# Kernel optimization log

Hardware: AMD Instinct MI355X
Metric: run time of the kernel (lower is better)

The kernel has to match this reference:

```python
import jax, jax.numpy as jnp
import numpy as np

B, S, D = 2, 2048, 1024
H, DK = 16, 64            # num_heads, d_kv; inner_dim = H*DK = 1024
NUM_BUCKETS = 32
MAX_DISTANCE = 128


def _relative_position_bucket(relative_position, bidirectional=True,
                              num_buckets=NUM_BUCKETS, max_distance=MAX_DISTANCE):
    # Faithful port of Mesh-TF / HF T5 bucketing (int32 in, int32 buckets out).
    relative_buckets = jnp.zeros_like(relative_position)
    if bidirectional:
        num_buckets = num_buckets // 2
        relative_buckets = relative_buckets + (relative_position > 0).astype(jnp.int32) * num_buckets
        relative_position = jnp.abs(relative_position)
    else:
        relative_position = -jnp.minimum(relative_position, 0)
    max_exact = num_buckets // 2
    is_small = relative_position < max_exact
    # log-spaced buckets for large distances; guard log(0) (masked by is_small anyway)
    rel_f = jnp.maximum(relative_position, 1).astype(jnp.float32)
    val_if_large = max_exact + (
        jnp.log(rel_f / max_exact) / np.log(max_distance / max_exact) * (num_buckets - max_exact)
    ).astype(jnp.int32)
    val_if_large = jnp.minimum(val_if_large, num_buckets - 1)
    return relative_buckets + jnp.where(is_small, relative_position, val_if_large)


def compute_bias(rel_emb, query_length, key_length):
    ctx = jnp.arange(query_length, dtype=jnp.int32)[:, None]
    mem = jnp.arange(key_length, dtype=jnp.int32)[None, :]
    buckets = _relative_position_bucket(mem - ctx, bidirectional=True)  # [q, k]
    values = rel_emb[buckets]                       # [q, k, H]
    return jnp.transpose(values, (2, 0, 1))[None]   # [1, H, q, k]


def setup_inputs() -> dict:
    key = jax.random.key(0)
    ks = jax.random.split(key, 6)
    scale = 1.0 / np.sqrt(D)
    return {
        "hidden_states": jax.random.normal(ks[0], (B, S, D), jnp.float32),
        "wq": jax.random.normal(ks[1], (D, H * DK), jnp.float32) * scale,
        "wk": jax.random.normal(ks[2], (D, H * DK), jnp.float32) * scale,
        "wv": jax.random.normal(ks[3], (D, H * DK), jnp.float32) * scale,
        "wo": jax.random.normal(ks[4], (H * DK, D), jnp.float32) * scale,
        "rel_emb": jax.random.normal(ks[5], (NUM_BUCKETS, H), jnp.float32),
    }


def reference(hidden_states, wq, wk, wv, wo, rel_emb):
    b, s, _ = hidden_states.shape

    def shape(x):  # [B,S,H*DK] -> [B,H,S,DK]
        return x.reshape(b, s, H, DK).transpose(0, 2, 1, 3)

    q = shape(hidden_states @ wq)   # NOTE: T5 does not scale q by 1/sqrt(d_kv)
    k = shape(hidden_states @ wk)
    v = shape(hidden_states @ wv)

    scores = jnp.einsum("bhqd,bhkd->bhqk", q, k)
    position_bias = compute_bias(rel_emb, s, s)     # [1,H,S,S]
    scores = scores + position_bias
    attn = jax.nn.softmax(scores, axis=-1)
    ctx = jnp.einsum("bhqk,bhkd->bhqd", attn, v)    # [B,H,S,DK]
    ctx = ctx.transpose(0, 2, 1, 3).reshape(b, s, H * DK)
    return ctx @ wo
```

## Files before the change

kernel.cpp:

```cpp
#include <hip/hip_runtime.h>


typedef __attribute__((ext_vector_type(8)))  unsigned short u16x8;
typedef __attribute__((ext_vector_type(4)))  unsigned short u16x4;
typedef __attribute__((ext_vector_type(8)))  __bf16         bf16x8;
typedef __attribute__((ext_vector_type(4)))  float          f32x4;
typedef __attribute__((ext_vector_type(4)))  unsigned int   u32x4;

#define GLOBAL_AS __attribute__((address_space(1)))
#define LDS_AS    __attribute__((address_space(3)))

static __device__ inline f32x4 MFMA(u16x8 a, u16x8 b, f32x4 c) {
  return __builtin_amdgcn_mfma_f32_16x16x32_bf16(
      __builtin_bit_cast(bf16x8, a), __builtin_bit_cast(bf16x8, b), c, 0, 0, 0);
}

static __device__ inline void gload16(const void* g, void* l) {
  __builtin_amdgcn_global_load_lds((const GLOBAL_AS unsigned int*)g,
                                   (LDS_AS unsigned int*)l, 16, 0, 0);
}

static __device__ inline unsigned short f2bf(float x) {
  unsigned int u = __builtin_bit_cast(unsigned int, x);
  u = (u + 0x7FFFu + ((u >> 16) & 1u)) >> 16;
  return (unsigned short)u;
}

static __device__ inline unsigned int cvtpk(float lo, float hi) {
  unsigned int r;
  asm volatile("v_cvt_pk_bf16_f32 %0, %1, %2" : "=v"(r) : "v"(lo), "v"(hi));
  return r;
}

static __device__ inline float max3f(float a, float b, float c) {
  float r;
  asm volatile("v_max3_f32 %0, %1, %2, %3" : "=v"(r) : "v"(a), "v"(b), "v"(c));
  return r;
}

#define L2E 1.4426950408889634f

__global__ __launch_bounds__(256) void k_prep(const float* __restrict__ hs,
                                              const float* __restrict__ wq,
                                              const float* __restrict__ wk,
                                              const float* __restrict__ wv,
                                              const float* __restrict__ wo,
                                              const float* __restrict__ re,
                                              unsigned short* __restrict__ hsb,
                                              unsigned short* __restrict__ wt,
                                              unsigned short* __restrict__ wot,
                                              float* __restrict__ btab) {
  __shared__ float tile[64][65];
  const int bid = blockIdx.x;
  const int t = threadIdx.x;

  if (bid < 4096) {
    int i = bid * 256 + t;
    float4 v = *(const float4*)(hs + (size_t)i * 4);
    u16x4 o;
    o[0] = f2bf(v.x); o[1] = f2bf(v.y); o[2] = f2bf(v.z); o[3] = f2bf(v.w);
    *(u16x4*)(hsb + (size_t)i * 4) = o;
  } else if (bid < 5120) {
    int sub = bid - 4096;
    int which = sub >> 8;
    int sb = sub & 255;
    int n0 = (sb & 15) << 6, k0 = (sb >> 4) << 6;
    const float* src = which == 0 ? wq : which == 1 ? wk : which == 2 ? wv : wo;
    unsigned short* dst = which == 0 ? wt
                        : which == 1 ? wt + 1048576
                        : which == 2 ? wt + 2097152 : wot;
    const int K = 1024, N = 1024;
    int rr = t >> 4, cc = (t & 15) << 2;
#pragma unroll
    for (int j = 0; j < 4; j++) {
      float4 v = *(const float4*)(src + (size_t)(k0 + rr + j * 16) * N + n0 + cc);
      tile[rr + j * 16][cc + 0] = v.x;
      tile[rr + j * 16][cc + 1] = v.y;
      tile[rr + j * 16][cc + 2] = v.z;
      tile[rr + j * 16][cc + 3] = v.w;
    }
    __syncthreads();
#pragma unroll
    for (int j = 0; j < 4; j++) {
      int n = rr + j * 16;
      u16x4 o;
      o[0] = f2bf(tile[cc + 0][n]);
      o[1] = f2bf(tile[cc + 1][n]);
      o[2] = f2bf(tile[cc + 2][n]);
      o[3] = f2bf(tile[cc + 3][n]);
      *(u16x4*)(dst + (size_t)(n0 + n) * K + k0 + cc) = o;
    }
  } else {
    int i = (bid - 5120) * 256 + t;
    if (i < 16 * 4095) {
      int h = i / 4095;
      int rp = i % 4095 - 2047;
      int rb = rp > 0 ? 16 : 0;
      int arp = rp < 0 ? -rp : rp;
      int v;
      if (arp < 8) {
        v = arp;
      } else {
        float tt = logf((float)arp * 0.125f);
        tt = tt / 2.772588722239781f;
        tt = tt * 8.0f;
        v = 8 + (int)tt;
        if (v > 15) v = 15;
      }
      btab[i] = re[(rb + v) * 16 + h] * L2E;
    }
  }
}

template <int EPI>
__global__ __launch_bounds__(256) void k_gemm(const unsigned short* __restrict__ A,
                                              const unsigned short* __restrict__ Bt,
                                              void* __restrict__ outp,
                                              int M, int N, int K) {
  __shared__ __attribute__((aligned(16))) char smem[32768];
  const int tid = threadIdx.x;
  const int lane = tid & 63, w = tid >> 6;
  const int l15 = lane & 15, g = lane >> 4;
  const int wr = w >> 1, wc = w & 1;
  const int bm0 = blockIdx.y << 7, bn0 = blockIdx.x << 7;

  const char* Ag = (const char*)A + (size_t)bm0 * K * 2;
  const char* Bg = (const char*)Bt + (size_t)bn0 * K * 2;

  f32x4 acc[4][4];
#pragma unroll
  for (int i = 0; i < 4; i++)
#pragma unroll
    for (int j = 0; j < 4; j++) acc[i][j] = (f32x4)0.0f;

  const int rowA = wr * 64 + l15;
  const int rowB = wc * 64 + l15;
  const int swz = (l15 & 7) << 4;

  for (int kt = 0; kt < K; kt += 64) {
#pragma unroll
    for (int j = 0; j < 4; j++) {
      int idx = ((j * 4 + w) << 10) + (lane << 4);
      int row = idx >> 7;
      int gs = (idx >> 4) & 7;
      size_t co = (size_t)row * (K * 2) + kt * 2 + ((gs ^ (row & 7)) << 4);
      gload16(Ag + co, smem + ((j * 4 + w) << 10));
      gload16(Bg + co, smem + 16384 + ((j * 4 + w) << 10));
    }
    __syncthreads();
#pragma unroll
    for (int kk = 0; kk < 2; kk++) {
      const int cp = ((kk << 6) + (g << 4)) ^ swz;
      u16x8 af[4], bfv[4];
#pragma unroll
      for (int mt = 0; mt < 4; mt++)
        af[mt] = *(const u16x8*)(smem + ((rowA + mt * 16) << 7) + cp);
#pragma unroll
      for (int nt = 0; nt < 4; nt++)
        bfv[nt] = *(const u16x8*)(smem + 16384 + ((rowB + nt * 16) << 7) + cp);
#pragma unroll
      for (int mt = 0; mt < 4; mt++)
#pragma unroll
        for (int nt = 0; nt < 4; nt++)
          acc[mt][nt] = MFMA(af[mt], bfv[nt], acc[mt][nt]);
    }
    __syncthreads();
  }

#pragma unroll
  for (int mt = 0; mt < 4; mt++) {
#pragma unroll
    for (int nt = 0; nt < 4; nt++) {
#pragma unroll
      for (int r = 0; r < 4; r++) {
        int m = bm0 + wr * 64 + mt * 16 + g * 4 + r;
        int n = bn0 + wc * 64 + nt * 16 + l15;
        float val = acc[mt][nt][r];
        if (EPI == 0) {
          int which = n >> 10;
          int hh = (n >> 6) & 15;
          int d = n & 63;
          int bb = m >> 11, s = m & 2047;
          int plane = bb * 16 + hh;
          unsigned short* o = (unsigned short*)outp;
          if (which == 0) {
            o[(size_t)plane * 131072 + (size_t)s * 64 + d] = f2bf(val * L2E);
          } else if (which == 1) {
            o[4194304 + (size_t)plane * 131072 + (size_t)s * 64 + d] = f2bf(val);
          } else {
            o[8388608 + (size_t)plane * 131072 + (size_t)d * 2048 + s] = f2bf(val);
          }
        } else {
          ((float*)outp)[(size_t)m * N + n] = val;
        }
      }
    }
  }
}

__global__ __launch_bounds__(256, 2) void k_attn(const unsigned short* __restrict__ qkv,
                                                 const float* __restrict__ btab,
                                                 unsigned short* __restrict__ ctx) {
  __shared__ __attribute__((aligned(16))) char smem[65536];
  const int tid = threadIdx.x;
  const int lane = tid & 63, w = tid >> 6;
  const int l15 = lane & 15, g = lane >> 4;

  const int wg = ((blockIdx.x & 7) << 6) + (blockIdx.x >> 3);
  const int plane = wg >> 4, qb = wg & 15;
  const int h = plane & 15, b = plane >> 4;
  const int q0w = (qb << 7) + (w << 5);

  const unsigned short* Qp = qkv + (size_t)plane * 131072;
  const unsigned short* Kp = qkv + 4194304 + (size_t)plane * 131072;
  const unsigned short* Vt = qkv + 8388608 + (size_t)plane * 131072;

  u16x8 qaA[2], qaB[2];
#pragma unroll
  for (int kk = 0; kk < 2; kk++) {
    qaA[kk] = *(const u16x8*)(Qp + (size_t)(q0w + l15) * 64 + kk * 32 + g * 8);
    qaB[kk] = *(const u16x8*)(Qp + (size_t)(q0w + 16 + l15) * 64 + kk * 32 + g * 8);
  }

  float m_rA = 0.0f, m_rB = 0.0f;
  f32x4 oaccA[4], oaccB[4], laccA, laccB;
#pragma unroll
  for (int t = 0; t < 4; t++) { oaccA[t] = (f32x4)0.0f; oaccB[t] = (f32x4)0.0f; }
  laccA = (f32x4)0.0f; laccB = (f32x4)0.0f;

  const float* browA = btab + h * 4095 + 2047 - q0w;
  const float* browB = browA - 16;
  const float cpos = btab[h * 4095 + 2047 + 1024];
  const float cneg = btab[h * 4095 + 2047 - 1024];

  u16x8 ones;
  {
    u32x4 ov = {0x3F803F80u, 0x3F803F80u, 0x3F803F80u, 0x3F803F80u};
    ones = __builtin_bit_cast(u16x8, ov);
  }

  const int srow = (w << 4) + (lane >> 3);
  const int soff = ((lane & 7) ^ (srow & 7)) << 4;
  const char* KsrcA = (const char*)Kp + (size_t)srow * 128 + soff;
  const char* KsrcB = KsrcA + 1024;
  const char* VsrcA = (const char*)Vt + (size_t)srow * 4096 + soff;
  const char* VsrcB = VsrcA + 32768;

  auto STAGE = [&](int t, int bsel) {
    char* sb = smem + (bsel << 14) + (w << 11);
    gload16(KsrcA + (size_t)t * 8192, sb);
    gload16(KsrcB + (size_t)t * 8192, sb + 1024);
    gload16(VsrcA + (size_t)t * 128, sb + 8192);
    gload16(VsrcB + (size_t)t * 128, sb + 8192 + 1024);
  };

  auto TILE = [&](int t, int bsel) {
    const char* kb = smem + (bsel << 14);
    const char* vbuf = kb + 8192;
    const int kv = t << 6;

    u16x8 kf[4][2], vf[4][2];
#pragma unroll
    for (int nt = 0; nt < 4; nt++) {
      int keyr = nt * 16 + l15;
      int sw = (keyr & 7) << 4;
      kf[nt][0] = *(const u16x8*)(kb + (keyr << 7) + ((g << 4) ^ sw));
      kf[nt][1] = *(const u16x8*)(kb + (keyr << 7) + ((64 + (g << 4)) ^ sw));
    }
#pragma unroll
    for (int tt = 0; tt < 4; tt++) {
      int d = tt * 16 + l15;
      int sw = (d & 7) << 4;
      vf[tt][0] = *(const u16x8*)(vbuf + (d << 7) + ((g << 4) ^ sw));
      vf[tt][1] = *(const u16x8*)(vbuf + (d << 7) + ((64 + (g << 4)) ^ sw));
    }

    auto FRAG = [&](const u16x8* qa, float& m_r, f32x4* oacc, f32x4& lacc,
                    const float* brow, int qf) {
      int delta_t = kv - qf;
      bool far = (delta_t >= 112 || delta_t <= -160);
      float cb = far ? (delta_t > 0 ? cpos : cneg) : 0.0f;
      float ebi = cb - m_r;
      f32x4 z0 = {ebi, ebi, ebi, ebi};

      f32x4 s[4];
      __builtin_amdgcn_s_setprio(1);
#pragma unroll
      for (int nt = 0; nt < 4; nt++) {
        f32x4 z = MFMA(kf[nt][0], qa[0], z0);
        z = MFMA(kf[nt][1], qa[1], z);
        s[nt] = z;
      }
      __builtin_amdgcn_s_setprio(0);

      if (!far) {
        const float* bp = brow + kv + (g << 2) - l15;
#pragma unroll
        for (int nt = 0; nt < 4; nt++)
#pragma unroll
          for (int r = 0; r < 4; r++) s[nt][r] += bp[nt * 16 + r];
      }

      float ma = max3f(s[0][0], s[0][1], s[0][2]);
      ma = max3f(ma, s[0][3], s[1][0]);
      ma = max3f(ma, s[1][1], s[1][2]);
      ma = fmaxf(ma, s[1][3]);
      float mb = max3f(s[2][0], s[2][1], s[2][2]);
      mb = max3f(mb, s[2][3], s[3][0]);
      mb = max3f(mb, s[3][1], s[3][2]);
      mb = fmaxf(mb, s[3][3]);
      float mloc = fmaxf(ma, mb);

      if (!__all(mloc <= 12.0f)) {
        float mxrow = fmaxf(mloc, __shfl_xor(mloc, 16));
        mxrow = fmaxf(mxrow, __shfl_xor(mxrow, 32));
        float dlt = fmaxf(mxrow, 0.0f);
        m_r += dlt;
        float alpha = exp2f(-dlt);
#pragma unroll
        for (int nt = 0; nt < 4; nt++)
#pragma unroll
          for (int r = 0; r < 4; r++) s[nt][r] -= dlt;
        float a4[4];
#pragma unroll
        for (int r = 0; r < 4; r++) a4[r] = __shfl(alpha, (g << 2) + r);
#pragma unroll
        for (int tt = 0; tt < 4; tt++) {
          f32x4 o = oacc[tt];
          o[0] *= a4[0]; o[1] *= a4[1]; o[2] *= a4[2]; o[3] *= a4[3];
          oacc[tt] = o;
        }
        lacc[0] *= a4[0]; lacc[1] *= a4[1]; lacc[2] *= a4[2]; lacc[3] *= a4[3];
      }

      unsigned int wpk[4][2];
#pragma unroll
      for (int nt = 0; nt < 4; nt++) {
#pragma unroll
        for (int r = 0; r < 4; r++)
          s[nt][r] = __builtin_amdgcn_exp2f(s[nt][r]);
        wpk[nt][0] = cvtpk(s[nt][0], s[nt][1]);
        wpk[nt][1] = cvtpk(s[nt][2], s[nt][3]);
      }
      u16x8 pa[2];
#pragma unroll
      for (int kk = 0; kk < 2; kk++) {
        unsigned int X0 = wpk[2 * kk][0], Y0 = wpk[2 * kk + 1][0];
        asm volatile("v_permlane32_swap_b32 %0, %1" : "+v"(X0), "+v"(Y0));
        asm volatile("v_permlane16_swap_b32 %0, %1" : "+v"(X0), "+v"(Y0));
        unsigned int X1 = wpk[2 * kk][1], Y1 = wpk[2 * kk + 1][1];
        asm volatile("v_permlane32_swap_b32 %0, %1" : "+v"(X1), "+v"(Y1));
        asm volatile("v_permlane16_swap_b32 %0, %1" : "+v"(X1), "+v"(Y1));
        u32x4 pw = {X0, X1, Y0, Y1};
        pa[kk] = __builtin_bit_cast(u16x8, pw);
      }

      __builtin_amdgcn_s_setprio(1);
#pragma unroll
      for (int tt = 0; tt < 4; tt++) {
        oacc[tt] = MFMA(pa[0], vf[tt][0], oacc[tt]);
        oacc[tt] = MFMA(pa[1], vf[tt][1], oacc[tt]);
      }
      lacc = MFMA(pa[0], ones, lacc);
      lacc = MFMA(pa[1], ones, lacc);
      __builtin_amdgcn_s_setprio(0);
    };

    FRAG(qaA, m_rA, oaccA, laccA, browA, q0w);
    __builtin_amdgcn_sched_barrier(0);
    FRAG(qaB, m_rB, oaccB, laccB, browB, q0w + 16);
  };

  STAGE(0, 0);
  STAGE(1, 1);
  __syncthreads();

  for (int it = 0; it < 16; ++it) {
    const int p  = (it & 1) << 1;
    const int sp = ((it + 1) & 1) << 1;
    if (it < 15) {
      STAGE(2 * it + 2, sp);
      STAGE(2 * it + 3, sp + 1);
    }
    TILE(2 * it, p);
    __builtin_amdgcn_sched_barrier(0);
    TILE(2 * it + 1, p + 1);
    __syncthreads();
  }

#pragma unroll
  for (int r = 0; r < 4; r++) {
    float inv = 1.0f / laccA[r];
    size_t rowoff = ((size_t)(b * 2048 + q0w + (g << 2) + r) << 10) + h * 64;
#pragma unroll
    for (int tt = 0; tt < 4; tt++)
      ctx[rowoff + tt * 16 + l15] = f2bf(oaccA[tt][r] * inv);
  }
#pragma unroll
  for (int r = 0; r < 4; r++) {
    float inv = 1.0f / laccB[r];
    size_t rowoff = ((size_t)(b * 2048 + q0w + 16 + (g << 2) + r) << 10) + h * 64;
#pragma unroll
    for (int tt = 0; tt < 4; tt++)
      ctx[rowoff + tt * 16 + l15] = f2bf(oaccB[tt][r] * inv);
  }
}

extern "C" void kernel_launch(void* const* d_in, const int* in_sizes, int n_in,
                              void* d_out, int out_size, void* d_ws, size_t ws_size,
                              hipStream_t stream) {
  const float* hs = (const float*)d_in[0];
  const float* wq = (const float*)d_in[1];
  const float* wk = (const float*)d_in[2];
  const float* wv = (const float*)d_in[3];
  const float* wo = (const float*)d_in[4];
  const float* re = (const float*)d_in[5];

  if (ws_size < 50593728u) return;

  char* ws = (char*)d_ws;
  unsigned short* hsb = (unsigned short*)(ws);
  unsigned short* wt  = (unsigned short*)(ws + 8388608);
  unsigned short* wot = (unsigned short*)(ws + 14680064);
  unsigned short* qkv = (unsigned short*)(ws + 16777216);
  unsigned short* ctx = (unsigned short*)(ws + 41943040);
  float*          btab = (float*)(ws + 50331648);

  k_prep<<<5376, 256, 0, stream>>>(hs, wq, wk, wv, wo, re, hsb, wt, wot, btab);
  k_gemm<0><<<dim3(24, 32), 256, 0, stream>>>(hsb, wt, qkv, 4096, 3072, 1024);
  k_attn<<<512, 256, 0, stream>>>(qkv, btab, ctx);
  k_gemm<1><<<dim3(8, 32), 256, 0, stream>>>(ctx, wot, d_out, 4096, 1024, 1024);
}
```

Before: 123.4 us.

## Split attention KV range across two wave groups and merge partial softmax

The attention block grows from 256 to 512 threads. Two halves of four waves each process the same 128 query rows over disjoint halves of the key sequence, each with its own double-buffered K/V LDS region. Afterwards the second half writes its output accumulators, row sums and running maxima to LDS, and the first half rescales and merges them flash-decoding style before normalising and storing. This aims to raise wave parallelism and latency hiding per query tile, at the cost of an extra LDS merge step and a launch bound that may squeeze registers and occupancy.

New measurement: 352.3 us. 185% more time.

```diff
diff --git a/kernel.cpp b/kernel.cpp
--- a/kernel.cpp
+++ b/kernel.cpp
@@ -198,18 +198,19 @@
   }
 }
 
-__global__ __launch_bounds__(256, 2) void k_attn(const unsigned short* __restrict__ qkv,
+__global__ __launch_bounds__(512, 4) void k_attn(const unsigned short* __restrict__ qkv,
                                                  const float* __restrict__ btab,
                                                  unsigned short* __restrict__ ctx) {
   __shared__ __attribute__((aligned(16))) char smem[65536];
   const int tid = threadIdx.x;
   const int lane = tid & 63, w = tid >> 6;
+  const int half = w >> 2, qg = w & 3;
   const int l15 = lane & 15, g = lane >> 4;
 
   const int wg = ((blockIdx.x & 7) << 6) + (blockIdx.x >> 3);
   const int plane = wg >> 4, qb = wg & 15;
   const int h = plane & 15, b = plane >> 4;
-  const int q0w = (qb << 7) + (w << 5);
+  const int q0w = (qb << 7) + (qg << 5);
 
   const unsigned short* Qp = qkv + (size_t)plane * 131072;
   const unsigned short* Kp = qkv + 4194304 + (size_t)plane * 131072;
@@ -239,25 +240,26 @@
     ones = __builtin_bit_cast(u16x8, ov);
   }
 
-  const int srow = (w << 4) + (lane >> 3);
+  const int srow = (qg << 4) + (lane >> 3);
   const int soff = ((lane & 7) ^ (srow & 7)) << 4;
   const char* KsrcA = (const char*)Kp + (size_t)srow * 128 + soff;
   const char* KsrcB = KsrcA + 1024;
   const char* VsrcA = (const char*)Vt + (size_t)srow * 4096 + soff;
   const char* VsrcB = VsrcA + 32768;
-
-  auto STAGE = [&](int t, int bsel) {
-    char* sb = smem + (bsel << 14) + (w << 11);
-    gload16(KsrcA + (size_t)t * 8192, sb);
-    gload16(KsrcB + (size_t)t * 8192, sb + 1024);
-    gload16(VsrcA + (size_t)t * 128, sb + 8192);
-    gload16(VsrcB + (size_t)t * 128, sb + 8192 + 1024);
+  char* const halfbase = smem + (half << 15);
+
+  auto STAGE = [&](int tile, int bsel) {
+    char* sb = halfbase + (bsel << 14) + (qg << 11);
+    gload16(KsrcA + (size_t)tile * 8192, sb);
+    gload16(KsrcB + (size_t)tile * 8192, sb + 1024);
+    gload16(VsrcA + (size_t)tile * 128, sb + 8192);
+    gload16(VsrcB + (size_t)tile * 128, sb + 8192 + 1024);
   };
 
-  auto TILE = [&](int t, int bsel) {
-    const char* kb = smem + (bsel << 14);
+  auto TILE = [&](int tile, int bsel) {
+    const char* kb = halfbase + (bsel << 14);
     const char* vbuf = kb + 8192;
-    const int kv = t << 6;
+    const int kv = tile << 6;
 
     u16x8 kf[4][2], vf[4][2];
 #pragma unroll
@@ -371,38 +373,79 @@
     FRAG(qaB, m_rB, oaccB, laccB, browB, q0w + 16);
   };
 
-  STAGE(0, 0);
-  STAGE(1, 1);
+  const int tbase = half << 4;
+  STAGE(tbase, 0);
   __syncthreads();
 
-  for (int it = 0; it < 16; ++it) {
-    const int p  = (it & 1) << 1;
-    const int sp = ((it + 1) & 1) << 1;
-    if (it < 15) {
-      STAGE(2 * it + 2, sp);
-      STAGE(2 * it + 3, sp + 1);
-    }
-    TILE(2 * it, p);
-    __builtin_amdgcn_sched_barrier(0);
-    TILE(2 * it + 1, p + 1);
+  for (int t = 0; t < 16; ++t) {
+    if (t < 15) STAGE(tbase + t + 1, (t + 1) & 1);
+    TILE(tbase + t, t & 1);
     __syncthreads();
   }
 
-#pragma unroll
-  for (int r = 0; r < 4; r++) {
-    float inv = 1.0f / laccA[r];
-    size_t rowoff = ((size_t)(b * 2048 + q0w + (g << 2) + r) << 10) + h * 64;
-#pragma unroll
-    for (int tt = 0; tt < 4; tt++)
-      ctx[rowoff + tt * 16 + l15] = f2bf(oaccA[tt][r] * inv);
-  }
-#pragma unroll
-  for (int r = 0; r < 4; r++) {
-    float inv = 1.0f / laccB[r];
-    size_t rowoff = ((size_t)(b * 2048 + q0w + 16 + (g << 2) + r) << 10) + h * 64;
-#pragma unroll
-    for (int tt = 0; tt < 4; tt++)
-      ctx[rowoff + tt * 16 + l15] = f2bf(oaccB[tt][r] * inv);
+  if (half == 1) {
+#pragma unroll
+    for (int tt = 0; tt < 4; tt++) {
+      *(f32x4*)(smem + ((((qg * 2 + 0) * 4 + tt) * 64 + lane) << 4)) = oaccA[tt];
+      *(f32x4*)(smem + ((((qg * 2 + 1) * 4 + tt) * 64 + lane) << 4)) = oaccB[tt];
+    }
+    *(f32x4*)(smem + 32768 + (((qg * 2 + 0) * 64 + lane) << 4)) = laccA;
+    *(f32x4*)(smem + 32768 + (((qg * 2 + 1) * 64 + lane) << 4)) = laccB;
+    *(float*)(smem + 40960 + (((qg * 2 + 0) * 64 + lane) << 2)) = m_rA;
+    *(float*)(smem + 40960 + (((qg * 2 + 1) * 64 + lane) << 2)) = m_rB;
+  }
+  __syncthreads();
+  if (half == 0) {
+    {
+      float pm = *(const float*)(smem + 40960 + (((qg * 2 + 0) * 64 + lane) << 2));
+      float ms = fmaxf(m_rA, pm);
+      float b0 = exp2f(m_rA - ms), b1 = exp2f(pm - ms);
+      float b0r[4], b1r[4];
+#pragma unroll
+      for (int r = 0; r < 4; r++) {
+        b0r[r] = __shfl(b0, (g << 2) + r);
+        b1r[r] = __shfl(b1, (g << 2) + r);
+      }
+      f32x4 pl = *(const f32x4*)(smem + 32768 + (((qg * 2 + 0) * 64 + lane) << 4));
+      float lm[4];
+#pragma unroll
+      for (int r = 0; r < 4; r++) lm[r] = laccA[r] * b0r[r] + pl[r] * b1r[r];
+#pragma unroll
+      for (int tt = 0; tt < 4; tt++) {
+        f32x4 po = *(const f32x4*)(smem + ((((qg * 2 + 0) * 4 + tt) * 64 + lane) << 4));
+#pragma unroll
+        for (int r = 0; r < 4; r++) {
+          float o = oaccA[tt][r] * b0r[r] + po[r] * b1r[r];
+          size_t row = (size_t)(b * 2048 + q0w + (g << 2) + r);
+          ctx[(row << 10) + h * 64 + tt * 16 + l15] = f2bf(o / lm[r]);
+        }
+      }
+    }
+    {
+      float pm = *(const float*)(smem + 40960 + (((qg * 2 + 1) * 64 + lane) << 2));
+      float ms = fmaxf(m_rB, pm);
+      float b0 = exp2f(m_rB - ms), b1 = exp2f(pm - ms);
+      float b0r[4], b1r[4];
+#pragma unroll
+      for (int r = 0; r < 4; r++) {
+        b0r[r] = __shfl(b0, (g << 2) + r);
+        b1r[r] = __shfl(b1, (g << 2) + r);
+      }
+      f32x4 pl = *(const f32x4*)(smem + 32768 + (((qg * 2 + 1) * 64 + lane) << 4));
+      float lm[4];
+#pragma unroll
+      for (int r = 0; r < 4; r++) lm[r] = laccB[r] * b0r[r] + pl[r] * b1r[r];
+#pragma unroll
+      for (int tt = 0; tt < 4; tt++) {
+        f32x4 po = *(const f32x4*)(smem + ((((qg * 2 + 1) * 4 + tt) * 64 + lane) << 4));
+#pragma unroll
+        for (int r = 0; r < 4; r++) {
+          float o = oaccB[tt][r] * b0r[r] + po[r] * b1r[r];
+          size_t row = (size_t)(b * 2048 + q0w + 16 + (g << 2) + r);
+          ctx[(row << 10) + h * 64 + tt * 16 + l15] = f2bf(o / lm[r]);
+        }
+      }
+    }
   }
 }
 
@@ -428,6 +471,6 @@
 
   k_prep<<<5376, 256, 0, stream>>>(hs, wq, wk, wv, wo, re, hsb, wt, wot, btab);
   k_gemm<0><<<dim3(24, 32), 256, 0, stream>>>(hsb, wt, qkv, 4096, 3072, 1024);
-  k_attn<<<512, 256, 0, stream>>>(qkv, btab, ctx);
+  k_attn<<<512, 512, 0, stream>>>(qkv, btab, ctx);
   k_gemm<1><<<dim3(8, 32), 256, 0, stream>>>(ctx, wot, d_out, 4096, 1024, 1024);
 }
```
